# Optimization experiments

Measured on AMD Instinct MI355X. Metric: run time of the kernel, lower is better.

## Reference

```python
import jax, jax.numpy as jnp
import numpy as np

N, C, L = 64, 3, 4096
K, S = 128, 64  # num_shapelets, shapelets_size


def setup_inputs() -> dict:
    key = jax.random.key(0)
    kx, ks = jax.random.split(key)
    x = jax.random.normal(kx, (N, C, L), dtype=jnp.float32)
    shapelets = jax.random.normal(ks, (C, K, S), dtype=jnp.float32)
    return {"x": x, "shapelets": shapelets}


def _min_euclid(x, shapelets):
    # x: (N, C, L); shapelets: (C, K, S)
    # Torch does unfold -> cdist -> min over windows -> min over channels.
    # We compute ||x_w - s||^2 = ||x_w||^2 + ||s||^2 - 2<x_w, s> with sliding
    # dot products via grouped 1-D conv (avoids materializing the unfold).
    C_, K_, S_ = shapelets.shape
    n = x.shape[0]
    filt = shapelets.reshape(C_ * K_, 1, S_)  # OIW, grouped by channel
    dots = jax.lax.conv_general_dilated(
        x, filt, window_strides=(1,), padding="VALID",
        dimension_numbers=("NCW", "OIW", "NCW"),
        feature_group_count=C_)                      # (N, C*K, W)
    ones = jnp.ones((C_, 1, S_), x.dtype)
    x2 = jax.lax.conv_general_dilated(
        x * x, ones, window_strides=(1,), padding="VALID",
        dimension_numbers=("NCW", "OIW", "NCW"),
        feature_group_count=C_)                      # (N, C, W) sliding ||x_w||^2
    W_ = dots.shape[-1]
    dots = dots.reshape(n, C_, K_, W_)               # (N, C, K, W)
    s2 = jnp.sum(shapelets * shapelets, axis=-1)     # (C, K)
    d2 = x2[:, :, None, :] + s2[None, :, :, None] - 2.0 * dots
    d = jnp.sqrt(jnp.maximum(d2, 0.0))               # Euclidean distance (N,C,K,W)
    d = jnp.min(d, axis=3)                           # min over windows -> (N, C, K)
    d = jnp.min(d, axis=1)                           # min over channels -> (N, K)
    return d[:, None, :]                             # (N, 1, K)


def reference(x, shapelets):
    return _min_euclid(x, shapelets)
```

## Files before the change

kernel.cpp:

```cpp
#include <hip/hip_runtime.h>
#include <hip/hip_bf16.h>

#define NN 64
#define CC 3
#define LL 4096
#define SS 64
#define KK 128
#define WW 4033
#define TILES 32
#define TPB 4
#define BLKN (TILES/TPB)

typedef __attribute__((ext_vector_type(8))) short v8s;
typedef __attribute__((ext_vector_type(4))) float v4f;

#define WS_CNT_OFF 32768
#define WS_HS2_OFF 33024
#define WS_SHB_OFF 34560
#define WS_HX2_OFF 131072

__device__ __forceinline__ unsigned bf16_rne(float f) {
    unsigned u = __float_as_uint(f);
    return (u + 0x7FFFu + ((u >> 16) & 1u)) >> 16;
}

__global__ __launch_bounds__(256) void me_prep(
        const float* __restrict__ x,
        const float* __restrict__ shp,
        unsigned* __restrict__ d2g,
        unsigned* __restrict__ cnt,
        float* __restrict__ hs2g,
        uint4* __restrict__ shb,
        float* __restrict__ hx2g) {
    const int b = blockIdx.x, t = threadIdx.x;
    if (b < NN * CC) {
        const int n = b / 3, c = b - n * 3;
        __shared__ float P[LL];
        __shared__ float wtot[4];
        const int lane = t & 63, wave = t >> 6;
        const float* xc = x + ((size_t)n * CC + c) * LL;
        const int base = t * 16;
        float q[16];
        {
            float4 A0 = *(const float4*)(xc + base);
            float4 A1 = *(const float4*)(xc + base + 4);
            float4 A2 = *(const float4*)(xc + base + 8);
            float4 A3 = *(const float4*)(xc + base + 12);
            q[0]=A0.x; q[1]=A0.y; q[2]=A0.z;  q[3]=A0.w;
            q[4]=A1.x; q[5]=A1.y; q[6]=A1.z;  q[7]=A1.w;
            q[8]=A2.x; q[9]=A2.y; q[10]=A2.z; q[11]=A2.w;
            q[12]=A3.x;q[13]=A3.y;q[14]=A3.z; q[15]=A3.w;
        }
        float run = 0.f;
        #pragma unroll
        for (int i = 0; i < 16; ++i) { run += q[i] * q[i]; q[i] = run; }
        float sc = run;
        #pragma unroll
        for (int d = 1; d < 64; d <<= 1) {
            float u = __shfl_up(sc, d, 64);
            if (lane >= d) sc += u;
        }
        if (lane == 63) wtot[wave] = sc;
        __syncthreads();
        float excl = sc - run;
        for (int w2 = 0; w2 < wave; ++w2) excl += wtot[w2];
        #pragma unroll
        for (int i = 0; i < 16; ++i) q[i] += excl;
        *(float4*)(P + base)      = make_float4(q[0], q[1], q[2], q[3]);
        *(float4*)(P + base + 4)  = make_float4(q[4], q[5], q[6], q[7]);
        *(float4*)(P + base + 8)  = make_float4(q[8], q[9], q[10], q[11]);
        *(float4*)(P + base + 12) = make_float4(q[12], q[13], q[14], q[15]);
        __syncthreads();
        float* dst = hx2g + ((size_t)n * CC + c) * LL;
        #pragma unroll
        for (int i = 0; i < 16; ++i) {
            int w = base + i;
            float o = -1e30f;
            if (w < WW) {
                float I1 = P[w + 63];
                float I0 = (w > 0) ? P[w - 1] : 0.f;
                o = -0.5f * (I1 - I0);
            }
            dst[w] = o;
        }
    } else {
        int tid = (b - NN * CC) * 256 + t;
        if (tid < NN * KK) d2g[tid] = 0x7F800000u;
        if (tid < NN) cnt[tid] = 0u;
        if (tid < CC * KK) {
            const float* r = shp + tid * SS;
            float a = 0.f;
            #pragma unroll 8
            for (int s = 0; s < SS; ++s) a += r[s] * r[s];
            hs2g[tid] = -0.5f * a;
        }
        if (tid < CC * 1024) {
            int c  = tid >> 10;
            int r  = tid & 1023;
            int nt = r >> 7;
            int scb = (r >> 6) & 1;
            int l  = r & 63;
            int row  = nt * 16 + (l & 15);
            int koff = scb * 32 + (l >> 4) * 8;
            const float* s = shp + ((size_t)(c * KK + row)) * SS + koff;
            float4 f0 = *(const float4*)s;
            float4 f1 = *(const float4*)(s + 4);
            uint4 o;
            o.x = (bf16_rne(f0.y) << 16) | bf16_rne(f0.x);
            o.y = (bf16_rne(f0.w) << 16) | bf16_rne(f0.z);
            o.z = (bf16_rne(f1.y) << 16) | bf16_rne(f1.x);
            o.w = (bf16_rne(f1.w) << 16) | bf16_rne(f1.z);
            shb[tid] = o;
        }
    }
}

__global__ __launch_bounds__(256, 2) void me_main(
        const float* __restrict__ x,
        const ushort* __restrict__ shb_g,
        const float* __restrict__ hs2g,
        const float* __restrict__ hx2g,
        unsigned* __restrict__ d2g,
        unsigned* __restrict__ cnt,
        float* __restrict__ out) {

    __shared__ __align__(16) ushort shb[CC * 8192];
    __shared__ ushort xs2[2][2][CC][200];
    __shared__ unsigned red[KK];
    __shared__ int lastflag;

    const int b    = blockIdx.x;
    const int n    = b >> 3;
    const int tg   = b & 7;
    const int t    = threadIdx.x;
    const int lane = t & 63, wave = t >> 6;
    const int quad = lane >> 4, col = lane & 15;
    const int wbase = wave * 32;

    if (t < KK) red[t] = 0x7F800000u;

    {
        typedef __attribute__((address_space(1))) const uint4 gu4;
        typedef __attribute__((address_space(3))) uint4 lu4;
        const uint4* gbase = (const uint4*)shb_g;
        #pragma unroll
        for (int it = 0; it < 12; ++it) {
            const uint4* gp = gbase + it * 256 + t;
            uint4* lp = (uint4*)shb + (it * 256 + wave * 64);
            __builtin_amdgcn_global_load_lds((gu4*)gp, (lu4*)lp, 16, 0, 0);
        }
    }

    float hsv[CC][8];
    #pragma unroll
    for (int c = 0; c < CC; ++c)
        #pragma unroll
        for (int nt = 0; nt < 8; ++nt)
            hsv[c][nt] = hs2g[c * KK + nt * 16 + col];

    const float* xb   = x + (size_t)n * (CC * LL);
    const float* hx2b = hx2g + (size_t)n * (CC * LL);

    float rmax[8];
    #pragma unroll
    for (int nt = 0; nt < 8; ++nt) rmax[nt] = -3.4e38f;

    for (int j = 0; j < TPB; ++j) {
        const int buf = j & 1;
        const int w0  = (tg * TPB + j) * 128;

        #pragma unroll
        for (int it = 0; it < 3; ++it) {
            int e = t + it * 256;
            if (e < 576) {
                int c = e / 192, idx = e - c * 192;
                int gi = w0 + idx;
                float vx = (gi < LL) ? xb[c * LL + gi] : 0.f;
                ushort hv = (ushort)bf16_rne(vx);
                xs2[buf][0][c][idx] = hv;
                if (idx > 0) xs2[buf][1][c][idx - 1] = hv;
            }
        }
        __syncthreads();

        #pragma unroll
        for (int c = 0; c < CC; ++c) {
            const float* hp = hx2b + c * LL + w0 + wbase + quad * 4;
            v4f hxv0 = *(const v4f*)(hp);
            v4f hxv1 = *(const v4f*)(hp + 16);
            v8s af[2][2];
            #pragma unroll
            for (int mt = 0; mt < 2; ++mt)
                #pragma unroll
                for (int sc = 0; sc < 2; ++sc) {
                    int e0 = wbase + mt * 16 + col + sc * 32 + quad * 8;
                    int p  = col & 1;
                    const uint* ap = (const uint*)&xs2[buf][p][c][e0 - p];
                    union { v8s v; uint u[4]; } au;
                    au.u[0] = ap[0]; au.u[1] = ap[1];
                    au.u[2] = ap[2]; au.u[3] = ap[3];
                    af[mt][sc] = au.v;
                }
            v4f acc[8][2];
            #pragma unroll
            for (int nt = 0; nt < 8; ++nt) {
                float h = hsv[c][nt];
                v4f a = {h, h, h, h};
                acc[nt][0] = a; acc[nt][1] = a;
            }
            #pragma unroll
            for (int sc = 0; sc < 2; ++sc)
                #pragma unroll
                for (int nt = 0; nt < 8; ++nt) {
                    v8s bfr = *(const v8s*)(shb + (((c * 8 + nt) * 2 + sc) * 64 + lane) * 8);
                    acc[nt][0] = __builtin_amdgcn_mfma_f32_16x16x32_bf16(af[0][sc], bfr, acc[nt][0], 0, 0, 0);
                    acc[nt][1] = __builtin_amdgcn_mfma_f32_16x16x32_bf16(af[1][sc], bfr, acc[nt][1], 0, 0, 0);
                }
            #pragma unroll
            for (int nt = 0; nt < 8; ++nt) {
                v4f a0 = acc[nt][0], a1 = acc[nt][1];
                float m = -3.4e38f;
                #pragma unroll
                for (int r = 0; r < 4; ++r)
                    m = fmaxf(m, fmaxf(a0[r] + hxv0[r], a1[r] + hxv1[r]));
                rmax[nt] = fmaxf(rmax[nt], m);
            }
        }
    }

    #pragma unroll
    for (int nt = 0; nt < 8; ++nt) {
        float v = rmax[nt];
        v = fmaxf(v, __shfl_xor(v, 16, 64));
        v = fmaxf(v, __shfl_xor(v, 32, 64));
        rmax[nt] = v;
    }
    if (quad == 0) {
        #pragma unroll
        for (int nt = 0; nt < 8; ++nt) {
            float d2 = fmaxf(-2.f * rmax[nt], 0.f);
            atomicMin(&red[nt * 16 + col], __float_as_uint(d2));
        }
    }
    __syncthreads();
    if (t < KK) atomicMin(&d2g[n * KK + t], red[t]);

    __syncthreads();
    if (t == 0) {
        unsigned old = atomicAdd(&cnt[n], 1u);
        lastflag = (old == BLKN - 1) ? 1 : 0;
    }
    __syncthreads();
    if (lastflag && t < KK) {
        unsigned bits = atomicMin(&d2g[n * KK + t], 0x7F800000u);
        out[n * KK + t] = sqrtf(__uint_as_float(bits));
    }
}

extern "C" void kernel_launch(void* const* d_in, const int* in_sizes, int n_in,
                              void* d_out, int out_size, void* d_ws, size_t ws_size,
                              hipStream_t stream) {
    const float* x   = (const float*)d_in[0];
    const float* shp = (const float*)d_in[1];
    unsigned* d2g  = (unsigned*)d_ws;
    unsigned* cnt  = (unsigned*)((char*)d_ws + WS_CNT_OFF);
    float*    hs2g = (float*)((char*)d_ws + WS_HS2_OFF);
    uint4*    shb  = (uint4*)((char*)d_ws + WS_SHB_OFF);
    float*    hx2g = (float*)((char*)d_ws + WS_HX2_OFF);
    float* out = (float*)d_out;

    hipLaunchKernelGGL(me_prep, dim3(NN * CC + 32), dim3(256), 0, stream,
                       x, shp, d2g, cnt, hs2g, shb, hx2g);
    hipLaunchKernelGGL(me_main, dim3(NN * TILES / TPB), dim3(256), 0, stream,
                       x, (const ushort*)shb, hs2g, hx2g, d2g, cnt, out);
}
```

Baseline: 79.40 us.

## Widen per-wave window tile to 64 and vectorize x staging loads

Each wave now handles 64 windows (four 16-row M tiles) instead of 32, so every shapelet B fragment read from LDS feeds four MFMAs instead of two. Each block processes two 256-window iterations instead of four 128-window ones. The staging of x into LDS moves from scalar to float4 loads with packed bf16 stores. The intent is to cut LDS traffic per MFMA and load instruction count. The cost is more live accumulator and A-fragment registers, which could limit occupancy at the existing launch bounds.

```diff
diff --git a/kernel.cpp b/kernel.cpp
--- a/kernel.cpp
+++ b/kernel.cpp
@@ -7,9 +7,7 @@
 #define SS 64
 #define KK 128
 #define WW 4033
-#define TILES 32
-#define TPB 4
-#define BLKN (TILES/TPB)
+#define BLKN 8
 
 typedef __attribute__((ext_vector_type(8))) short v8s;
 typedef __attribute__((ext_vector_type(4))) float v4f;
@@ -95,11 +93,11 @@
             hs2g[tid] = -0.5f * a;
         }
         if (tid < CC * 1024) {
-            int c  = tid >> 10;
-            int r  = tid & 1023;
-            int nt = r >> 7;
+            int c   = tid >> 10;
+            int r   = tid & 1023;
+            int nt  = r >> 7;
             int scb = (r >> 6) & 1;
-            int l  = r & 63;
+            int l   = r & 63;
             int row  = nt * 16 + (l & 15);
             int koff = scb * 32 + (l >> 4) * 8;
             const float* s = shp + ((size_t)(c * KK + row)) * SS + koff;
@@ -125,7 +123,7 @@
         float* __restrict__ out) {
 
     __shared__ __align__(16) ushort shb[CC * 8192];
-    __shared__ ushort xs2[2][2][CC][200];
+    __shared__ __align__(8) ushort xs2[2][2][CC][320];
     __shared__ unsigned red[KK];
     __shared__ int lastflag;
 
@@ -135,7 +133,7 @@
     const int t    = threadIdx.x;
     const int lane = t & 63, wave = t >> 6;
     const int quad = lane >> 4, col = lane & 15;
-    const int wbase = wave * 32;
+    const int wbase = wave * 64;
 
     if (t < KK) red[t] = 0x7F800000u;
 
@@ -165,32 +163,40 @@
     #pragma unroll
     for (int nt = 0; nt < 8; ++nt) rmax[nt] = -3.4e38f;
 
-    for (int j = 0; j < TPB; ++j) {
-        const int buf = j & 1;
-        const int w0  = (tg * TPB + j) * 128;
-
-        #pragma unroll
-        for (int it = 0; it < 3; ++it) {
-            int e = t + it * 256;
-            if (e < 576) {
-                int c = e / 192, idx = e - c * 192;
-                int gi = w0 + idx;
-                float vx = (gi < LL) ? xb[c * LL + gi] : 0.f;
-                ushort hv = (ushort)bf16_rne(vx);
-                xs2[buf][0][c][idx] = hv;
-                if (idx > 0) xs2[buf][1][c][idx - 1] = hv;
+    for (int it = 0; it < 2; ++it) {
+        const int buf = it;
+        const int w0  = tg * 512 + it * 256;
+
+        if (t < 240) {
+            int c = t / 80, q = t - c * 80;
+            int idx = q * 4, gi = w0 + idx;
+            float4 v;
+            if (gi + 3 < LL) v = *(const float4*)(xb + c * LL + gi);
+            else {
+                v.x = (gi     < LL) ? xb[c * LL + gi]     : 0.f;
+                v.y = (gi + 1 < LL) ? xb[c * LL + gi + 1] : 0.f;
+                v.z = (gi + 2 < LL) ? xb[c * LL + gi + 2] : 0.f;
+                v.w = (gi + 3 < LL) ? xb[c * LL + gi + 3] : 0.f;
             }
+            unsigned h0 = bf16_rne(v.x), h1 = bf16_rne(v.y);
+            unsigned h2 = bf16_rne(v.z), h3 = bf16_rne(v.w);
+            uint2 p0; p0.x = h0 | (h1 << 16); p0.y = h2 | (h3 << 16);
+            *(uint2*)&xs2[buf][0][c][idx] = p0;
+            if (idx > 0) xs2[buf][1][c][idx - 1] = (ushort)h0;
+            *(uint*)&xs2[buf][1][c][idx] = h1 | (h2 << 16);
+            xs2[buf][1][c][idx + 2] = (ushort)h3;
         }
         __syncthreads();
 
         #pragma unroll
         for (int c = 0; c < CC; ++c) {
             const float* hp = hx2b + c * LL + w0 + wbase + quad * 4;
-            v4f hxv0 = *(const v4f*)(hp);
-            v4f hxv1 = *(const v4f*)(hp + 16);
-            v8s af[2][2];
+            v4f hxv[4];
             #pragma unroll
-            for (int mt = 0; mt < 2; ++mt)
+            for (int mt = 0; mt < 4; ++mt) hxv[mt] = *(const v4f*)(hp + mt * 16);
+            v8s af[4][2];
+            #pragma unroll
+            for (int mt = 0; mt < 4; ++mt)
                 #pragma unroll
                 for (int sc = 0; sc < 2; ++sc) {
                     int e0 = wbase + mt * 16 + col + sc * 32 + quad * 8;
@@ -201,29 +207,39 @@
                     au.u[2] = ap[2]; au.u[3] = ap[3];
                     af[mt][sc] = au.v;
                 }
-            v4f acc[8][2];
             #pragma unroll
-            for (int nt = 0; nt < 8; ++nt) {
-                float h = hsv[c][nt];
-                v4f a = {h, h, h, h};
-                acc[nt][0] = a; acc[nt][1] = a;
-            }
-            #pragma unroll
-            for (int sc = 0; sc < 2; ++sc)
-                #pragma unroll
-                for (int nt = 0; nt < 8; ++nt) {
-                    v8s bfr = *(const v8s*)(shb + (((c * 8 + nt) * 2 + sc) * 64 + lane) * 8);
-                    acc[nt][0] = __builtin_amdgcn_mfma_f32_16x16x32_bf16(af[0][sc], bfr, acc[nt][0], 0, 0, 0);
-                    acc[nt][1] = __builtin_amdgcn_mfma_f32_16x16x32_bf16(af[1][sc], bfr, acc[nt][1], 0, 0, 0);
+            for (int g = 0; g < 2; ++g) {
+                v4f acc[4][4];
+                #pragma unroll
+                for (int nt2 = 0; nt2 < 4; ++nt2) {
+                    float h = hsv[c][g * 4 + nt2];
+                    v4f a = {h, h, h, h};
+                    #pragma unroll
+                    for (int mt = 0; mt < 4; ++mt) acc[nt2][mt] = a;
                 }
-            #pragma unroll
-            for (int nt = 0; nt < 8; ++nt) {
-                v4f a0 = acc[nt][0], a1 = acc[nt][1];
-                float m = -3.4e38f;
-                #pragma unroll
-                for (int r = 0; r < 4; ++r)
-                    m = fmaxf(m, fmaxf(a0[r] + hxv0[r], a1[r] + hxv1[r]));
-                rmax[nt] = fmaxf(rmax[nt], m);
+                #pragma unroll
+                for (int sc = 0; sc < 2; ++sc)
+                    #pragma unroll
+                    for (int nt2 = 0; nt2 < 4; ++nt2) {
+                        int nt = g * 4 + nt2;
+                        v8s bfr = *(const v8s*)(shb + (((c * 8 + nt) * 2 + sc) * 64 + lane) * 8);
+                        #pragma unroll
+                        for (int mt = 0; mt < 4; ++mt)
+                            acc[nt2][mt] = __builtin_amdgcn_mfma_f32_16x16x32_bf16(
+                                af[mt][sc], bfr, acc[nt2][mt], 0, 0, 0);
+                    }
+                #pragma unroll
+                for (int nt2 = 0; nt2 < 4; ++nt2) {
+                    float m = -3.4e38f;
+                    #pragma unroll
+                    for (int mt = 0; mt < 4; ++mt) {
+                        v4f a = acc[nt2][mt];
+                        #pragma unroll
+                        for (int r = 0; r < 4; ++r)
+                            m = fmaxf(m, a[r] + hxv[mt][r]);
+                    }
+                    rmax[g * 4 + nt2] = fmaxf(rmax[g * 4 + nt2], m);
+                }
             }
         }
     }
@@ -271,6 +287,6 @@
 
     hipLaunchKernelGGL(me_prep, dim3(NN * CC + 32), dim3(256), 0, stream,
                        x, shp, d2g, cnt, hs2g, shb, hx2g);
-    hipLaunchKernelGGL(me_main, dim3(NN * TILES / TPB), dim3(256), 0, stream,
+    hipLaunchKernelGGL(me_main, dim3(NN * BLKN), dim3(256), 0, stream,
                        x, (const ushort*)shb, hs2g, hx2g, d2g, cnt, out);
 }
```

New measurement: 76.92 us, median of 2. 3.1% less time.
